# Optimization experiments

Measured on AMD Instinct MI355X. Metric: run time of the kernel, lower is better.

The kernel has to match this reference:

```python
import math
import jax, jax.numpy as jnp
import numpy as np

FNUM = 64      # exp_channels (fnum)
NHEADS = 4     # num_heads
WS = 8         # window size (both spatial dims)
SHIFT = 4      # cyclic shift (hard-coded in module)
SCALE = FNUM ** -0.5   # NOTE: module scales by fnum**-0.5, not head_dim**-0.5
LN_EPS = 1e-5


def sine_pos_encoding(h, w, num_pos_feats, temperature=10000.0):
    # DETR-style normalized sine position encoding -> (1, h*w, 2*num_pos_feats)
    scale = 2.0 * math.pi
    y = np.cumsum(np.ones((1, h, w), dtype=np.float64), axis=1)
    x = np.cumsum(np.ones((1, h, w), dtype=np.float64), axis=2)
    eps = 1e-6
    y = y / (y[:, -1:, :] + eps) * scale
    x = x / (x[:, :, -1:] + eps) * scale
    dim_t = np.arange(num_pos_feats, dtype=np.float64)
    dim_t = temperature ** (2.0 * (dim_t // 2) / num_pos_feats)
    pos_x = x[..., None] / dim_t
    pos_y = y[..., None] / dim_t
    pos_x = np.stack([np.sin(pos_x[..., 0::2]), np.cos(pos_x[..., 1::2])], axis=-1).reshape(1, h, w, -1)
    pos_y = np.stack([np.sin(pos_y[..., 0::2]), np.cos(pos_y[..., 1::2])], axis=-1).reshape(1, h, w, -1)
    pos = np.concatenate([pos_y, pos_x], axis=-1)
    return jnp.asarray(pos.reshape(1, h * w, 2 * num_pos_feats), dtype=jnp.float32)


def compute_mask_np(H, W, ws, ss):
    # Swin shifted-window attention mask -> (nW, ws*ws, ws*ws) with 0 / -100
    img = np.zeros((H, W))
    cnt = 0
    for hs in (slice(0, -ws), slice(-ws, -ss), slice(-ss, None)):
        for wsl in (slice(0, -ws), slice(-ws, -ss), slice(-ss, None)):
            img[hs, wsl] = cnt
            cnt += 1
    mw = img.reshape(H // ws, ws, W // ws, ws).transpose(0, 2, 1, 3).reshape(-1, ws * ws)
    diff = mw[:, None, :] - mw[:, :, None]
    return jnp.asarray(np.where(diff != 0, -100.0, 0.0), dtype=jnp.float32)


def layernorm(x, w, b):
    m = x.mean(-1, keepdims=True)
    v = x.var(-1, keepdims=True)
    return (x - m) * jax.lax.rsqrt(v + LN_EPS) * w + b


def window_attention(q, k, v, mask):
    # q,k,v: (Bw, nH, N, Ch); mask: (nW, N, N)
    att = jnp.einsum('bhnc,bhmc->bhnm', q * SCALE, k)
    nW, N = mask.shape[0], mask.shape[1]
    att = att.reshape(-1, nW, NHEADS, N, N) + mask[None, :, None]
    att = jax.nn.softmax(att.reshape(-1, NHEADS, N, N), axis=-1)
    out = jnp.einsum('bhnm,bhmc->bnhc', att, v)   # merge heads as (nH C)
    return out.reshape(out.shape[0], N, -1)


def merge_heads(q):
    # (Bw, nH, N, Ch) -> (Bw, N, nH*Ch)
    return q.transpose(0, 2, 1, 3).reshape(q.shape[0], q.shape[2], -1)


def geglu(h, w11, b11, w12, b12, w2, b2):
    return (jax.nn.gelu(h @ w11 + b11, approximate=False) * (h @ w12 + b12)) @ w2 + b2


def reference(x, ln1_w, ln1_b, ln2_w, ln2_b, w_qkv, me_w11, me_b11, me_w12, me_b12, me_w2, me_b2, conv11_w, ff_in_w, ff_dw_w, ff_out_w):
    B, _, C, H, W = x.shape
    nHw, nWw = H // WS, W // WS
    nW = nHw * nWw
    N = WS * WS
    Ch = FNUM // NHEADS
    pos = sine_pos_encoding(WS, WS, FNUM // 2)
    mask = compute_mask_np(H, W, WS, SHIFT)
    x0 = x
    xs = jnp.roll(x, (-SHIFT, -SHIFT), axis=(3, 4))
    # window partition: (B,3,C,H,W) -> (B*3*nW, N, C)
    xw = xs.reshape(B, 3, C, nHw, WS, nWw, WS).transpose(0, 1, 3, 5, 4, 6, 2).reshape(-1, N, C)
    xw = layernorm(xw, ln1_w, ln1_b)
    qkv = (xw + pos) @ w_qkv                                   # (B*3*nW, N, 3F)
    # '(B E nW) W (nP C) -> E nP (B nW) W C'
    qkv = qkv.reshape(B, 3, nW, N, 3, FNUM).transpose(1, 4, 0, 2, 3, 5).reshape(3, 3, B * nW, N, FNUM)
    # '(C nH)' head split: head index is the fast axis (faithful to source)
    qkv = qkv.reshape(3, 3, B * nW, N, Ch, NHEADS).transpose(0, 1, 2, 5, 3, 4)  # (E, P, Bw, nH, N, Ch)
    a1 = window_attention(qkv[1, 0], qkv[0, 1], qkv[0, 2], mask)
    a3 = window_attention(qkv[1, 0], qkv[2, 1], qkv[2, 2], mask)
    a21 = window_attention(qkv[0, 0], qkv[1, 1], qkv[1, 2], mask)
    a21b = window_attention(qkv[0, 0], qkv[2, 1], qkv[2, 2], mask)
    a23 = window_attention(qkv[2, 0], qkv[1, 1], qkv[1, 2], mask)
    a23b = window_attention(qkv[2, 0], qkv[0, 1], qkv[0, 2], mask)
    # keep_query=True path: concat attended features with own query, GEGLU per exposure
    h1 = geglu(jnp.concatenate([a21, a21b, merge_heads(qkv[0, 0])], -1), me_w11[0], me_b11[0], me_w12[0], me_b12[0], me_w2[0], me_b2[0])
    h2 = geglu(jnp.concatenate([a1, a3, merge_heads(qkv[1, 0])], -1), me_w11[1], me_b11[1], me_w12[1], me_b12[1], me_w2[1], me_b2[1])
    h3 = geglu(jnp.concatenate([a23, a23b, merge_heads(qkv[2, 0])], -1), me_w11[2], me_b11[2], me_w12[2], me_b12[2], me_w2[2], me_b2[2])
    xc = jnp.concatenate([h1, h2, h3], 0)                      # (3*B*nW, N, F)
    # window reverse + ffn_dconv 1x1 conv across 3F channels
    xr = xc.reshape(3, B, nHw, nWw, WS, WS, FNUM).transpose(1, 0, 6, 2, 4, 3, 5).reshape(B, 3 * FNUM, H, W)
    xr = jnp.einsum('oi,bihw->bohw', conv11_w, xr).reshape(B, 3, FNUM, H, W)
    xr = jnp.roll(xr, (SHIFT, SHIFT), axis=(3, 4))
    xres = xr + x0
    # FFN: LN over (N C), then GEGLU dwconv FeedForward
    xl = layernorm(xres.transpose(0, 3, 4, 1, 2).reshape(B, H, W, 3 * FNUM), ln2_w, ln2_b)
    xcn = xl.transpose(0, 3, 1, 2)                             # (B, 3F, H, W)
    h = jnp.einsum('oi,bihw->bohw', ff_in_w, xcn)              # (B, 12F, H, W)
    h = jax.lax.conv_general_dilated(h, ff_dw_w[:, None], (1, 1), ((1, 1), (1, 1)),
                                     feature_group_count=h.shape[1],
                                     dimension_numbers=('NCHW', 'OIHW', 'NCHW'))
    g1, g2 = jnp.split(h, 2, axis=1)
    h = jax.nn.gelu(g1, approximate=False) * g2                # (B, 6F, H, W)
    out = jnp.einsum('oi,bihw->bohw', ff_out_w, h).reshape(B, 3, FNUM, H, W)
    return xres + out


def setup_inputs():
    key = jax.random.key(0)
    ks = jax.random.split(key, 10)
    F3, F6, F12 = 3 * FNUM, 6 * FNUM, 12 * FNUM
    def w(k, shape, fan_in):
        return jax.random.normal(k, shape, jnp.float32) * (fan_in ** -0.5)
    return {
        'x': jax.random.normal(ks[0], (1, 3, FNUM, 256, 256), jnp.float32),
        'ln1_w': jnp.ones((FNUM,), jnp.float32),
        'ln1_b': jnp.zeros((FNUM,), jnp.float32),
        'ln2_w': jnp.ones((F3,), jnp.float32),
        'ln2_b': jnp.zeros((F3,), jnp.float32),
        'w_qkv': w(ks[1], (FNUM, F3), FNUM),
        'me_w11': w(ks[2], (3, F3, FNUM), F3),
        'me_b11': jnp.zeros((3, FNUM), jnp.float32),
        'me_w12': w(ks[3], (3, F3, FNUM), F3),
        'me_b12': jnp.zeros((3, FNUM), jnp.float32),
        'me_w2': w(ks[4], (3, FNUM, FNUM), FNUM),
        'me_b2': jnp.zeros((3, FNUM), jnp.float32),
        'conv11_w': w(ks[5], (F3, F3), F3),
        'ff_in_w': w(ks[6], (F12, F3), F3),
        'ff_dw_w': w(ks[7], (F12, 3, 3), 9),
        'ff_out_w': w(ks[8], (F3, F6), F6),
    }
```

## Files before the change

kernel.cpp:

```cpp
#include <hip/hip_runtime.h>
#include <hip/hip_bf16.h>
#include <math.h>

typedef __hip_bfloat16 bf16;
typedef __attribute__((ext_vector_type(8))) short short8;
typedef __attribute__((ext_vector_type(4))) short short4v;
typedef __attribute__((ext_vector_type(4))) float f32x4;

__device__ __forceinline__ float b2f(bf16 v) { return __bfloat162float(v); }
__device__ __forceinline__ bf16 f2b(float v) { return __float2bfloat16(v); }
__device__ __forceinline__ short f2s(float v) { bf16 b = __float2bfloat16(v); return *(short*)&b; }
__device__ __forceinline__ float s2f(short s) { bf16 b = *(bf16*)&s; return __bfloat162float(b); }
__device__ __forceinline__ float gelu_exact(float x) {
  return 0.5f * x * (1.0f + erff(x * 0.7071067811865476f));
}
__device__ __forceinline__ bool detect_f32(const void* ln1w) {
  return *(const unsigned int*)ln1w == 0x3F800000u;
}
__device__ __forceinline__ float ldx(const void* p, int i, bool f32) {
  return f32 ? ((const float*)p)[i] : b2f(((const bf16*)p)[i]);
}
#define MFMA16(a, b, c) __builtin_amdgcn_mfma_f32_16x16x32_bf16((a), (b), (c), 0, 0, 0)

#define OFF_LN1W  0
#define OFF_LN1B  64
#define OFF_LN2W  128
#define OFF_LN2B  320
#define OFF_WQKVT 512
#define OFF_W11T  12800
#define OFF_B11   49664
#define OFF_W12T  49856
#define OFF_B12   86720
#define OFF_W2T   86912
#define OFF_B2    99200
#define OFF_CW    99392
#define OFF_FIW   136256
#define OFF_DWW   283712
#define OFF_FOW   290624

__global__ void __launch_bounds__(256) k_convert(
    const void* __restrict__ src, bf16* __restrict__ dst, int n,
    const void* __restrict__ raw) {
  const bool f32 = detect_f32(raw);
  int i = blockIdx.x * 256 + threadIdx.x;
  if (i < n) dst[i] = f2b(ldx(src, i, f32));
}

__global__ void __launch_bounds__(256) k_convT(
    const void* __restrict__ src, bf16* __restrict__ dst, int R, int C, int n,
    const void* __restrict__ raw) {
  const bool f32 = detect_f32(raw);
  int i = blockIdx.x * 256 + threadIdx.x;
  if (i >= n) return;
  int rc = R * C;
  int s = i / rc, rem = i - s * rc;
  int r = rem / C, c = rem - r * C;
  dst[s * rc + c * R + r] = f2b(ldx(src, i, f32));
}

__global__ void __launch_bounds__(256) k_pos(float* __restrict__ posT) {
  int i = blockIdx.x * 256 + threadIdx.x;
  if (i >= 4096) return;
  int t = i >> 6, ch = i & 63;
  int r = t >> 3, c = t & 7;
  int c2 = ch & 31;
  float coord = (ch < 32) ? (float)(r + 1) : (float)(c + 1);
  float base = coord * (6.283185307179586f / 8.000001f);
  int k = c2 >> 1;
  float d = powf(10000.0f, (float)k * (1.0f / 16.0f));
  float a = base / d;
  posT[i] = (c2 & 1) ? cosf(a) : sinf(a);
}

__global__ void __launch_bounds__(256) k_qkv(
    const void* __restrict__ x, const void* __restrict__ raw,
    const bf16* __restrict__ W, const float* __restrict__ posT,
    short* __restrict__ qkvS, int wy0, int NWL) {
  const int wl = blockIdx.x;
  const int wy = wy0 + (wl >> 5), wx = wl & 31;
  const int tid = threadIdx.x;
  const bool xf32 = detect_f32(raw);

  __shared__ alignas(16) short xln[192 * 72];
  __shared__ alignas(16) short qout[64 * 200];
  __shared__ float mu[192], rs[192];

  for (int i = tid; i < 3072; i += 256) {
    int xq = i & 1, ty = (i >> 1) & 7, ch = (i >> 4) & 63, e = i >> 10;
    int y  = (wy * 8 + ty + 4) & 255;
    int xs = (wx * 8 + 4 + xq * 4) & 255;
    size_t gi = ((size_t)(e * 64 + ch) * 256 + y) * 256 + xs;
    float f0, f1, f2, f3;
    if (xf32) {
      f32x4 v4 = *(const f32x4*)((const float*)x + gi);
      f0 = v4[0]; f1 = v4[1]; f2 = v4[2]; f3 = v4[3];
    } else {
      short4v v4 = *(const short4v*)((const bf16*)x + gi);
      f0 = s2f(v4[0]); f1 = s2f(v4[1]); f2 = s2f(v4[2]); f3 = s2f(v4[3]);
    }
    int tb = (e * 64 + ty * 8 + xq * 4) * 72 + ch;
    xln[tb]       = f2s(f0);
    xln[tb + 72]  = f2s(f1);
    xln[tb + 144] = f2s(f2);
    xln[tb + 216] = f2s(f3);
  }
  __syncthreads();
  if (tid < 192) {
    const short* row = xln + tid * 72;
    float s = 0.f, s2 = 0.f;
    #pragma unroll
    for (int k8 = 0; k8 < 8; k8++) {
      short8 v = *(const short8*)(row + k8 * 8);
      #pragma unroll
      for (int j = 0; j < 8; j++) { float f = s2f(v[j]); s += f; s2 += f * f; }
    }
    float m = s * (1.0f / 64.0f);
    float var = s2 * (1.0f / 64.0f) - m * m;
    mu[tid] = m; rs[tid] = rsqrtf(var + 1e-5f);
  }
  __syncthreads();
  for (int u = tid; u < 1536; u += 256) {
    int co = u & 7, t = (u >> 3) & 63, e = u >> 9;
    int idx = (e * 64 + t) * 72 + co * 8;
    short8 xv = *(const short8*)(xln + idx);
    float m = mu[e * 64 + t], rr = rs[e * 64 + t];
    const float* pt = posT + t * 64 + co * 8;
    f32x4 pa = *(const f32x4*)pt;
    f32x4 pb = *(const f32x4*)(pt + 4);
    short8 lw = *(const short8*)(const void*)(W + OFF_LN1W + co * 8);
    short8 lb = *(const short8*)(const void*)(W + OFF_LN1B + co * 8);
    short8 o;
    #pragma unroll
    for (int j = 0; j < 8; j++) {
      float p = (j < 4) ? pa[j] : pb[j - 4];
      o[j] = f2s((s2f(xv[j]) - m) * rr * s2f(lw[j]) + s2f(lb[j]) + p);
    }
    *(short8*)(xln + idx) = o;
  }
  __syncthreads();

  const int lid = tid & 63;
  const int w = tid >> 6;
  const int mrow = lid & 15, q = lid >> 4;
  const bf16* wqT = W + OFF_WQKVT;
  for (int e = 0; e < 3; e++) {
    short8 a0 = *(const short8*)(xln + (e * 64 + w * 16 + mrow) * 72 + q * 8);
    short8 a1 = *(const short8*)(xln + (e * 64 + w * 16 + mrow) * 72 + 32 + q * 8);
    for (int nt = 0; nt < 12; nt++) {
      f32x4 acc = {0.f, 0.f, 0.f, 0.f};
      short8 b0 = *(const short8*)(const void*)(wqT + (nt * 16 + mrow) * 64 + q * 8);
      short8 b1 = *(const short8*)(const void*)(wqT + (nt * 16 + mrow) * 64 + 32 + q * 8);
      acc = MFMA16(a0, b0, acc);
      acc = MFMA16(a1, b1, acc);
      #pragma unroll
      for (int r = 0; r < 4; r++)
        qout[(w * 16 + q * 4 + r) * 200 + nt * 16 + mrow] = f2s(acc[r]);
    }
    __syncthreads();
    for (int i = tid; i < 3072; i += 256) {
      int p = i >> 10, rem = i & 1023;
      int tt = rem >> 4, f4 = (rem & 15) * 4;
      *(short4v*)(qkvS + ((size_t)wl * 9 + e * 3 + p) * 4096 + tt * 64 + f4)
          = *(const short4v*)(qout + tt * 200 + p * 64 + f4);
    }
    __syncthreads();
  }
}

__global__ void __launch_bounds__(256, 3) k_attn(
    const short* __restrict__ qkvS, const bf16* __restrict__ W,
    short* __restrict__ xcS, int wy0, int NWL) {
  const int e  = blockIdx.x / NWL;
  const int wl = blockIdx.x - e * NWL;
  const int wy = wy0 + (wl >> 5), wx = wl & 31;
  const int tid = threadIdx.x;

  __shared__ alignas(16) short cat[64 * 200];
  __shared__ alignas(16) short Kh[4 * 64 * 16];
  __shared__ alignas(16) short Vt[4 * 16 * 72];
  __shared__ alignas(16) short Pb[64 * 72];
  short* gbuf = Pb;

  const int ea = (e == 0) ? 1 : ((e == 1) ? 0 : 1);
  const int eb = (e == 0) ? 2 : ((e == 1) ? 2 : 0);
  const short* Qg = qkvS + ((size_t)wl * 9 + e * 3 + 0) * 4096;
  const short* Kg[2] = { qkvS + ((size_t)wl * 9 + ea * 3 + 1) * 4096,
                         qkvS + ((size_t)wl * 9 + eb * 3 + 1) * 4096 };
  const short* Vg[2] = { qkvS + ((size_t)wl * 9 + ea * 3 + 2) * 4096,
                         qkvS + ((size_t)wl * 9 + eb * 3 + 2) * 4096 };

  for (int i = tid; i < 512; i += 256) {
    int t = i >> 3, chunk = i & 7;
    short8 v = *(const short8*)(Qg + t * 64 + chunk * 8);
    #pragma unroll
    for (int j = 0; j < 8; j++) {
      int f = chunk * 8 + j;
      cat[t * 200 + 128 + (f & 3) * 16 + (f >> 2)] = v[j];
    }
  }

  const int lid = tid & 63;
  const int w = tid >> 6;
  const int mrow = lid & 15, q = lid >> 4;
  const int masky = (wy == 31), maskx = (wx == 31);
  const short8 zero8 = {0, 0, 0, 0, 0, 0, 0, 0};

  for (int src = 0; src < 2; src++) {
    if (src) __syncthreads();
    for (int i = tid; i < 512; i += 256) {
      int t = i >> 3, chunk = i & 7;
      short8 v = *(const short8*)(Kg[src] + t * 64 + chunk * 8);
      #pragma unroll
      for (int j = 0; j < 8; j++) {
        int f = chunk * 8 + j;
        Kh[((f & 3) * 64 + t) * 16 + (f >> 2)] = v[j];
      }
    }
    for (int i = tid; i < 512; i += 256) {
      int t = i & 63, chunk = i >> 6;
      short8 v = *(const short8*)(Vg[src] + t * 64 + chunk * 8);
      #pragma unroll
      for (int j = 0; j < 8; j++) {
        int f = chunk * 8 + j;
        Vt[((f & 3) * 16 + (f >> 2)) * 72 + t] = v[j];
      }
    }
    __syncthreads();

    for (int h = 0; h < 4; h++) {
      short8 af = (q < 2)
          ? *(const short8*)(cat + (w * 16 + mrow) * 200 + 128 + h * 16 + q * 8) : zero8;
      f32x4 s[4];
      #pragma unroll
      for (int nt = 0; nt < 4; nt++) {
        short8 bfr = (q < 2)
            ? *(const short8*)(Kh + (h * 64 + nt * 16 + mrow) * 16 + q * 8) : zero8;
        f32x4 acc = {0.f, 0.f, 0.f, 0.f};
        s[nt] = MFMA16(af, bfr, acc);
      }
      #pragma unroll
      for (int nt = 0; nt < 4; nt++) {
        int kj = nt * 16 + mrow;
        int lyj = masky ? (((kj >> 3) < 4) ? 1 : 2) : 0;
        int lxj = maskx ? (((kj & 7) < 4) ? 1 : 2) : 0;
        #pragma unroll
        for (int r = 0; r < 4; r++) {
          int qi = w * 16 + q * 4 + r;
          int lyi = masky ? (((qi >> 3) < 4) ? 1 : 2) : 0;
          int lxi = maskx ? (((qi & 7) < 4) ? 1 : 2) : 0;
          float sv = s[nt][r] * 0.125f;
          if (lyi != lyj || lxi != lxj) sv -= 100.0f;
          s[nt][r] = sv;
        }
      }
      #pragma unroll
      for (int r = 0; r < 4; r++) {
        float mx = fmaxf(fmaxf(s[0][r], s[1][r]), fmaxf(s[2][r], s[3][r]));
        mx = fmaxf(mx, __shfl_xor(mx, 1));
        mx = fmaxf(mx, __shfl_xor(mx, 2));
        mx = fmaxf(mx, __shfl_xor(mx, 4));
        mx = fmaxf(mx, __shfl_xor(mx, 8));
        float p0 = __expf(s[0][r] - mx), p1 = __expf(s[1][r] - mx);
        float p2 = __expf(s[2][r] - mx), p3 = __expf(s[3][r] - mx);
        float sum = (p0 + p1) + (p2 + p3);
        sum += __shfl_xor(sum, 1);
        sum += __shfl_xor(sum, 2);
        sum += __shfl_xor(sum, 4);
        sum += __shfl_xor(sum, 8);
        float inv = 1.0f / sum;
        int ro = (w * 16 + q * 4 + r) * 72;
        Pb[ro + mrow]      = f2s(p0 * inv);
        Pb[ro + 16 + mrow] = f2s(p1 * inv);
        Pb[ro + 32 + mrow] = f2s(p2 * inv);
        Pb[ro + 48 + mrow] = f2s(p3 * inv);
      }
      asm volatile("s_waitcnt lgkmcnt(0)" ::: "memory");
      f32x4 o = {0.f, 0.f, 0.f, 0.f};
      #pragma unroll
      for (int kc = 0; kc < 2; kc++) {
        short8 pa = *(const short8*)(Pb + (w * 16 + mrow) * 72 + kc * 32 + q * 8);
        short8 vb = *(const short8*)(Vt + (h * 16 + mrow) * 72 + kc * 32 + q * 8);
        o = MFMA16(pa, vb, o);
      }
      #pragma unroll
      for (int r = 0; r < 4; r++)
        cat[(w * 16 + q * 4 + r) * 200 + src * 64 + h * 16 + mrow] = f2s(o[r]);
    }
  }
  __syncthreads();

  {
    short8 a[6];
    #pragma unroll
    for (int kc = 0; kc < 6; kc++)
      a[kc] = *(const short8*)(cat + (w * 16 + mrow) * 200 + kc * 32 + q * 8);
    f32x4 ua[4], va[4];
    const bf16* w1T = W + OFF_W11T + (size_t)e * 64 * 192;
    const bf16* w2T = W + OFF_W12T + (size_t)e * 64 * 192;
    for (int nt = 0; nt < 4; nt++) {
      f32x4 au = {0.f, 0.f, 0.f, 0.f}, av = {0.f, 0.f, 0.f, 0.f};
      #pragma unroll
      for (int kc = 0; kc < 6; kc++) {
        short8 bu = *(const short8*)(const void*)(w1T + (nt * 16 + mrow) * 192 + kc * 32 + q * 8);
        short8 bv = *(const short8*)(const void*)(w2T + (nt * 16 + mrow) * 192 + kc * 32 + q * 8);
        au = MFMA16(a[kc], bu, au);
        av = MFMA16(a[kc], bv, av);
      }
      ua[nt] = au; va[nt] = av;
    }
    for (int nt = 0; nt < 4; nt++) {
      int o = nt * 16 + mrow;
      float bu = b2f(W[OFF_B11 + e * 64 + o]);
      float bv = b2f(W[OFF_B12 + e * 64 + o]);
      #pragma unroll
      for (int r = 0; r < 4; r++)
        gbuf[(w * 16 + q * 4 + r) * 72 + o] = f2s(gelu_exact(ua[nt][r] + bu) * (va[nt][r] + bv));
    }
  }
  {
    short8 g0 = *(const short8*)(gbuf + (w * 16 + mrow) * 72 + q * 8);
    short8 g1 = *(const short8*)(gbuf + (w * 16 + mrow) * 72 + 32 + q * 8);
    const bf16* w2T = W + OFF_W2T + (size_t)e * 64 * 64;
    for (int nt = 0; nt < 4; nt++) {
      f32x4 acc = {0.f, 0.f, 0.f, 0.f};
      short8 b0 = *(const short8*)(const void*)(w2T + (nt * 16 + mrow) * 64 + q * 8);
      short8 b1 = *(const short8*)(const void*)(w2T + (nt * 16 + mrow) * 64 + 32 + q * 8);
      acc = MFMA16(g0, b0, acc);
      acc = MFMA16(g1, b1, acc);
      int o = nt * 16 + mrow;
      float bb = b2f(W[OFF_B2 + e * 64 + o]);
      #pragma unroll
      for (int r = 0; r < 4; r++)
        cat[(w * 16 + q * 4 + r) * 200 + o] = f2s(acc[r] + bb);
    }
  }
  __syncthreads();
  short* xcbase = xcS + ((size_t)wl * 3 + e) * 4096;
  for (int i = tid; i < 1024; i += 256) {
    int tt = i >> 4, f4 = (i & 15) * 4;
    *(short4v*)(xcbase + tt * 64 + f4) = *(const short4v*)(cat + tt * 200 + f4);
  }
}

__global__ void __launch_bounds__(256) k_conv11(
    const short* __restrict__ xcS, const bf16* __restrict__ W,
    const void* __restrict__ x, const void* __restrict__ raw,
    short* __restrict__ xres, int wy0, int NWL) {
  const int wl = blockIdx.x;
  const int wy = wy0 + (wl >> 5), wx = wl & 31;
  const int tid = threadIdx.x;
  const bool xf32 = detect_f32(raw);
  __shared__ alignas(16) short ct[64 * 200];
  __shared__ alignas(16) short xt[64 * 200];

  for (int i = tid; i < 3072; i += 256) {
    int e = i >> 10, rem = i & 1023;
    int tt = rem >> 4, f4 = (rem & 15) * 4;
    *(short4v*)(ct + tt * 200 + e * 64 + f4)
        = *(const short4v*)(xcS + ((size_t)wl * 3 + e) * 4096 + tt * 64 + f4);
  }
  for (int i = tid; i < 3072; i += 256) {
    int xq = i & 1, ty = (i >> 1) & 7, ch = (i >> 4) & 63, e = i >> 10;
    int y  = (wy * 8 + ty + 4) & 255;
    int xs = (wx * 8 + 4 + xq * 4) & 255;
    size_t gi = ((size_t)(e * 64 + ch) * 256 + y) * 256 + xs;
    float f0, f1, f2, f3;
    if (xf32) {
      f32x4 v4 = *(const f32x4*)((const float*)x + gi);
      f0 = v4[0]; f1 = v4[1]; f2 = v4[2]; f3 = v4[3];
    } else {
      short4v v4 = *(const short4v*)((const bf16*)x + gi);
      f0 = s2f(v4[0]); f1 = s2f(v4[1]); f2 = s2f(v4[2]); f3 = s2f(v4[3]);
    }
    int tb = (ty * 8 + xq * 4) * 200 + e * 64 + ch;
    xt[tb]       = f2s(f0);
    xt[tb + 200] = f2s(f1);
    xt[tb + 400] = f2s(f2);
    xt[tb + 600] = f2s(f3);
  }
  __syncthreads();

  const int lid = tid & 63;
  const int w = tid >> 6;
  const int mrow = lid & 15, q = lid >> 4;
  short8 a[6];
  #pragma unroll
  for (int kc = 0; kc < 6; kc++)
    a[kc] = *(const short8*)(ct + (w * 16 + mrow) * 200 + kc * 32 + q * 8);
  __syncthreads();

  const bf16* cw = W + OFF_CW;
  for (int nt = 0; nt < 12; nt++) {
    f32x4 acc = {0.f, 0.f, 0.f, 0.f};
    #pragma unroll
    for (int kc = 0; kc < 6; kc++) {
      short8 b = *(const short8*)(const void*)(cw + (nt * 16 + mrow) * 192 + kc * 32 + q * 8);
      acc = MFMA16(a[kc], b, acc);
    }
    int o = nt * 16 + mrow;
    #pragma unroll
    for (int r = 0; r < 4; r++) {
      int t = w * 16 + q * 4 + r;
      ct[t * 200 + o] = f2s(acc[r] + s2f(xt[t * 200 + o]));
    }
  }
  __syncthreads();
  for (int i4 = tid; i4 < 3072; i4 += 256) {
    int t = i4 / 48, o4 = (i4 - t * 48) * 4;
    int y  = (wy * 8 + (t >> 3) + 4) & 255;
    int xx = (wx * 8 + (t & 7) + 4) & 255;
    *(short4v*)(xres + (size_t)(y * 256 + xx) * 192 + o4)
        = *(const short4v*)(ct + t * 200 + o4);
  }
}

__global__ void __launch_bounds__(256) k_ffin(
    const short* __restrict__ xres, const bf16* __restrict__ W,
    short* __restrict__ hS, int y_start, int y0m1) {
  const int y = y_start + (blockIdx.x >> 2);
  const int x0 = (blockIdx.x & 3) * 64;
  const int l = y - y0m1;
  const int tid = threadIdx.x;
  __shared__ alignas(16) short xt[64 * 200];
  __shared__ float mu[64], rs[64];

  for (int i4 = tid; i4 < 3072; i4 += 256) {
    int p = i4 / 48, c4 = (i4 - p * 48) * 4;
    *(short4v*)(xt + p * 200 + c4)
        = *(const short4v*)(xres + (size_t)(y * 256 + x0 + p) * 192 + c4);
  }
  __syncthreads();
  {
    int p = tid >> 2, qd = tid & 3;
    const short* row = xt + p * 200 + qd * 48;
    float s = 0.f, s2 = 0.f;
    #pragma unroll
    for (int k = 0; k < 6; k++) {
      short8 v = *(const short8*)(row + k * 8);
      #pragma unroll
      for (int j = 0; j < 8; j++) { float f = s2f(v[j]); s += f; s2 += f * f; }
    }
    s  += __shfl_xor(s, 1);  s  += __shfl_xor(s, 2);
    s2 += __shfl_xor(s2, 1); s2 += __shfl_xor(s2, 2);
    if (qd == 0) {
      float m = s * (1.0f / 192.0f);
      float var = s2 * (1.0f / 192.0f) - m * m;
      mu[p] = m; rs[p] = rsqrtf(var + 1e-5f);
    }
  }
  __syncthreads();
  for (int i = tid; i < 12288; i += 256) {
    int p = i & 63, ch = i >> 6;
    int idx = p * 200 + ch;
    xt[idx] = f2s((s2f(xt[idx]) - mu[p]) * rs[p] * b2f(W[OFF_LN2W + ch]) + b2f(W[OFF_LN2B + ch]));
  }
  __syncthreads();

  const int lid = tid & 63;
  const int m0 = (tid >> 6) * 16;
  const int mrow = lid & 15, q = lid >> 4;
  short8 a[6];
  #pragma unroll
  for (int kc = 0; kc < 6; kc++)
    a[kc] = *(const short8*)(xt + (m0 + mrow) * 200 + kc * 32 + q * 8);
  __syncthreads();

  const bf16* fiw = W + OFF_FIW;
  for (int c = 0; c < 4; c++) {
    for (int j = 0; j < 12; j++) {
      int nt = c * 12 + j;
      f32x4 acc = {0.f, 0.f, 0.f, 0.f};
      #pragma unroll
      for (int kc = 0; kc < 6; kc++) {
        short8 b = *(const short8*)(const void*)(fiw + (nt * 16 + mrow) * 192 + kc * 32 + q * 8);
        acc = MFMA16(a[kc], b, acc);
      }
      #pragma unroll
      for (int r = 0; r < 4; r++)
        xt[(m0 + q * 4 + r) * 200 + j * 16 + mrow] = f2s(acc[r]);
    }
    __syncthreads();
    for (int i4 = tid; i4 < 3072; i4 += 256) {
      int t = i4 / 48, o4 = (i4 - t * 48) * 4;
      *(short4v*)(hS + (size_t)l * 196608 + (size_t)(x0 + t) * 768 + c * 192 + o4)
          = *(const short4v*)(xt + t * 200 + o4);
    }
    __syncthreads();
  }
}

__global__ void __launch_bounds__(256) k_ffout(
    const short* __restrict__ hS, const bf16* __restrict__ W,
    const short* __restrict__ xres, void* __restrict__ out,
    const void* __restrict__ raw, int y0, int y0m1) {
  const int y = y0 + (blockIdx.x >> 2);
  const int x0 = (blockIdx.x & 3) * 64;
  const int tid = threadIdx.x;
  const bool of32 = detect_f32(raw);
  __shared__ alignas(16) short ga[64 * 392];

  const bf16* dwwT = W + OFF_DWW;
  const int l = y - y0m1;
  const short8 z8 = {0, 0, 0, 0, 0, 0, 0, 0};
  for (int it = 0; it < 6; it++) {
    int unit = it * 256 + tid;
    int pq = unit / 48, oo = unit - pq * 48;
    int o = oo * 8;
    int xxb = x0 + pq * 2;
    float u0[8] = {0,0,0,0,0,0,0,0}, v0[8] = {0,0,0,0,0,0,0,0};
    float u1[8] = {0,0,0,0,0,0,0,0}, v1[8] = {0,0,0,0,0,0,0,0};
    #pragma unroll
    for (int dy = -1; dy <= 1; dy++) {
      int yy = y + dy;
      if (yy < 0 || yy >= 256) continue;
      const short* rbase = hS + (size_t)(l + dy) * 196608;
      short8 hu[4], hv[4];
      #pragma unroll
      for (int k = 0; k < 4; k++) {
        int xv = xxb - 1 + k;
        if (xv < 0 || xv >= 256) { hu[k] = z8; hv[k] = z8; }
        else {
          const short* hp = rbase + (size_t)xv * 768 + o;
          hu[k] = *(const short8*)(hp);
          hv[k] = *(const short8*)(hp + 384);
        }
      }
      const bf16* wrow = dwwT + (dy + 1) * 3 * 768 + o;
      short8 w0u = *(const short8*)(const void*)(wrow);
      short8 w0v = *(const short8*)(const void*)(wrow + 384);
      short8 w1u = *(const short8*)(const void*)(wrow + 768);
      short8 w1v = *(const short8*)(const void*)(wrow + 768 + 384);
      short8 w2u = *(const short8*)(const void*)(wrow + 1536);
      short8 w2v = *(const short8*)(const void*)(wrow + 1536 + 384);
      #pragma unroll
      for (int j = 0; j < 8; j++) {
        float a0 = s2f(w0u[j]), a1 = s2f(w1u[j]), a2 = s2f(w2u[j]);
        float b0 = s2f(w0v[j]), b1 = s2f(w1v[j]), b2 = s2f(w2v[j]);
        float h0u = s2f(hu[0][j]), h1u = s2f(hu[1][j]), h2u = s2f(hu[2][j]), h3u = s2f(hu[3][j]);
        float h0v = s2f(hv[0][j]), h1v = s2f(hv[1][j]), h2v = s2f(hv[2][j]), h3v = s2f(hv[3][j]);
        u0[j] += a0 * h0u + a1 * h1u + a2 * h2u;
        u1[j] += a0 * h1u + a1 * h2u + a2 * h3u;
        v0[j] += b0 * h0v + b1 * h1v + b2 * h2v;
        v1[j] += b0 * h1v + b1 * h2v + b2 * h3v;
      }
    }
    short8 g0, g1;
    #pragma unroll
    for (int j = 0; j < 8; j++) {
      g0[j] = f2s(gelu_exact(u0[j]) * v0[j]);
      g1[j] = f2s(gelu_exact(u1[j]) * v1[j]);
    }
    *(short8*)(ga + (pq * 2) * 392 + o)     = g0;
    *(short8*)(ga + (pq * 2 + 1) * 392 + o) = g1;
  }
  __syncthreads();

  const int lid = tid & 63;
  const int m0 = (tid >> 6) * 16;
  const int mrow = lid & 15, q = lid >> 4;
  short8 a[12];
  #pragma unroll
  for (int kc = 0; kc < 12; kc++)
    a[kc] = *(const short8*)(ga + (m0 + mrow) * 392 + kc * 32 + q * 8);
  __syncthreads();

  for (int i4 = tid; i4 < 3072; i4 += 256) {
    int pp = i4 / 48, c4 = (i4 - pp * 48) * 4;
    *(short4v*)(ga + pp * 392 + 200 + c4)
        = *(const short4v*)(xres + (size_t)(y * 256 + x0 + pp) * 192 + c4);
  }

  const bf16* fow = W + OFF_FOW;
  for (int nt = 0; nt < 12; nt++) {
    f32x4 acc = {0.f, 0.f, 0.f, 0.f};
    #pragma unroll
    for (int kc = 0; kc < 12; kc++) {
      short8 b = *(const short8*)(const void*)(fow + (nt * 16 + mrow) * 384 + kc * 32 + q * 8);
      acc = MFMA16(a[kc], b, acc);
    }
    #pragma unroll
    for (int r = 0; r < 4; r++)
      ga[(m0 + q * 4 + r) * 392 + nt * 16 + mrow] = f2s(acc[r]);
  }
  __syncthreads();

  for (int it = 0; it < 48; it++) {
    int flat = it * 256 + tid;
    int pp = flat & 63, ch = flat >> 6;
    int idx = ch * 65536 + y * 256 + x0 + pp;
    float r = s2f(ga[pp * 392 + ch]) + s2f(ga[pp * 392 + 200 + ch]);
    if (of32) ((float*)out)[idx] = r;
    else      ((bf16*)out)[idx] = f2b(r);
  }
}

extern "C" void kernel_launch(void* const* d_in, const int* in_sizes, int n_in,
                              void* d_out, int out_size, void* d_ws, size_t ws_size,
                              hipStream_t stream) {
  const void* x   = d_in[0];
  const void* raw = d_in[1];
  char* ws = (char*)d_ws;
  bf16*  W    = (bf16*)(ws + 1024);
  float* posT = (float*)(ws + 786432);
  short* xres = (short*)(ws + 0x100000);
  const size_t ATT = 28ull * 1024 * 1024;

  size_t avail = (ws_size > ATT) ? ws_size - ATT : 0;
  int swr = 32;
  while (swr > 1 && (size_t)swr * 3145728ull > avail) swr >>= 1;
  int hr = 256;
  while (hr > 4 && (size_t)(hr + 2) * 393216ull > avail) hr >>= 1;

  short* qkvS = (short*)(ws + ATT);
  short* xcS  = (short*)(ws + ATT + (size_t)swr * 2359296ull);
  short* hS   = (short*)(ws + ATT);

  { const int di[10]   = {1, 2, 3, 4, 7, 9, 11, 12, 13, 15};
    const int offp[10] = {OFF_LN1W, OFF_LN1B, OFF_LN2W, OFF_LN2B, OFF_B11,
                          OFF_B12, OFF_B2, OFF_CW, OFF_FIW, OFF_FOW};
    const int cnt[10]  = {64, 64, 192, 192, 192, 192, 192, 36864, 147456, 73728};
    for (int i = 0; i < 10; i++)
      k_convert<<<(cnt[i] + 255) / 256, 256, 0, stream>>>(
          d_in[di[i]], W + offp[i], cnt[i], raw);
  }
  k_convT<<<(12288 + 255) / 256, 256, 0, stream>>>(d_in[5], W + OFF_WQKVT, 64, 192, 12288, raw);
  k_convT<<<(36864 + 255) / 256, 256, 0, stream>>>(d_in[6], W + OFF_W11T, 192, 64, 36864, raw);
  k_convT<<<(36864 + 255) / 256, 256, 0, stream>>>(d_in[8], W + OFF_W12T, 192, 64, 36864, raw);
  k_convT<<<(12288 + 255) / 256, 256, 0, stream>>>(d_in[10], W + OFF_W2T, 64, 64, 12288, raw);
  k_convT<<<(6912 + 255) / 256, 256, 0, stream>>>(d_in[14], W + OFF_DWW, 768, 9, 6912, raw);
  k_pos<<<16, 256, 0, stream>>>(posT);

  for (int wy0 = 0; wy0 < 32; wy0 += swr) {
    int NWL = swr * 32;
    k_qkv<<<NWL, 256, 0, stream>>>(x, raw, W, posT, qkvS, wy0, NWL);
    k_attn<<<3 * NWL, 256, 0, stream>>>(qkvS, W, xcS, wy0, NWL);
    k_conv11<<<NWL, 256, 0, stream>>>(xcS, W, x, raw, xres, wy0, NWL);
  }

  for (int y0 = 0; y0 < 256; y0 += hr) {
    int ys = (y0 == 0) ? 0 : (y0 - 1);
    int ye = (y0 + hr > 255) ? 255 : (y0 + hr);
    int nrows = ye - ys + 1;
    k_ffin<<<nrows * 4, 256, 0, stream>>>(xres, W, hS, ys, y0 - 1);
    k_ffout<<<hr * 4, 256, 0, stream>>>(hS, W, xres, d_out, raw, y0, y0 - 1);
  }
}
```

Before: 741.8 us.

## Pre-layout QKV per head for attention, transpose score MFMA, widen depthwise tiles

The QKV kernel now writes Q, K (pre-scaled by 0.125) and V in head-split, attention-ready layouts, so the attention kernel can copy them with vector loads instead of scalar scatter transposes. Attention computes the transposed score product, so each lane holds a full query row. That turns the softmax reductions into two shuffles and lets probabilities be stored as short4 vectors. The shift mask is precomputed once per thread and applied only on edge windows. Separately, the depthwise FFN stage computes four output pixels per thread instead of two to reuse loaded neighbours, with launch bounds set for three blocks per SM, at the cost of higher register pressure.

```diff
diff --git a/kernel.cpp b/kernel.cpp
--- a/kernel.cpp
+++ b/kernel.cpp
@@ -38,6 +38,10 @@
 #define OFF_DWW   283712
 #define OFF_FOW   290624
 
+#define QOFF 0
+#define KOFF 4352
+#define VOFF 9472
+
 __global__ void __launch_bounds__(256) k_convert(
     const void* __restrict__ src, bf16* __restrict__ dst, int n,
     const void* __restrict__ raw) {
@@ -82,7 +86,7 @@
   const bool xf32 = detect_f32(raw);
 
   __shared__ alignas(16) short xln[192 * 72];
-  __shared__ alignas(16) short qout[64 * 200];
+  __shared__ alignas(16) short qout[13824];
   __shared__ float mu[192], rs[192];
 
   for (int i = tid; i < 3072; i += 256) {
@@ -142,6 +146,8 @@
   const int lid = tid & 63;
   const int w = tid >> 6;
   const int mrow = lid & 15, q = lid >> 4;
+  const int t0 = w * 16 + q * 4;
+  const int h = mrow & 3;
   const bf16* wqT = W + OFF_WQKVT;
   for (int e = 0; e < 3; e++) {
     short8 a0 = *(const short8*)(xln + (e * 64 + w * 16 + mrow) * 72 + q * 8);
@@ -152,16 +158,33 @@
       short8 b1 = *(const short8*)(const void*)(wqT + (nt * 16 + mrow) * 64 + 32 + q * 8);
       acc = MFMA16(a0, b0, acc);
       acc = MFMA16(a1, b1, acc);
-      #pragma unroll
-      for (int r = 0; r < 4; r++)
-        qout[(w * 16 + q * 4 + r) * 200 + nt * 16 + mrow] = f2s(acc[r]);
+      int p = nt >> 2;
+      int c = (nt & 3) * 4 + (mrow >> 2);
+      if (p == 0) {
+        int o2 = h * 16 + c;
+        #pragma unroll
+        for (int r = 0; r < 4; r++)
+          qout[QOFF + (t0 + r) * 68 + o2] = f2s(acc[r]);
+      } else if (p == 1) {
+        int rb = KOFF + (h * 64 + t0) * 20 + c;
+        #pragma unroll
+        for (int r = 0; r < 4; r++)
+          qout[rb + r * 20] = f2s(acc[r] * 0.125f);
+      } else {
+        int rb = VOFF + (h * 16 + c) * 68 + q * 16 + w;
+        #pragma unroll
+        for (int r = 0; r < 4; r++)
+          qout[rb + r * 4] = f2s(acc[r]);
+      }
     }
     __syncthreads();
-    for (int i = tid; i < 3072; i += 256) {
-      int p = i >> 10, rem = i & 1023;
-      int tt = rem >> 4, f4 = (rem & 15) * 4;
-      *(short4v*)(qkvS + ((size_t)wl * 9 + e * 3 + p) * 4096 + tt * 64 + f4)
-          = *(const short4v*)(qout + tt * 200 + p * 64 + f4);
+    const size_t gb = ((size_t)wl * 9 + e * 3) * 4096;
+    for (int u = tid; u < 3072; u += 256) {
+      int j = u * 4, p = j >> 12, rem = j & 4095, src;
+      if (p == 0)      src = QOFF + (rem >> 6) * 68 + (rem & 63);
+      else if (p == 1) src = KOFF + (rem >> 4) * 20 + (rem & 15);
+      else             src = VOFF + (rem >> 6) * 68 + (rem & 63);
+      *(short4v*)(qkvS + gb + j) = *(const short4v*)(qout + src);
     }
     __syncthreads();
   }
@@ -176,9 +199,10 @@
   const int tid = threadIdx.x;
 
   __shared__ alignas(16) short cat[64 * 200];
-  __shared__ alignas(16) short Kh[4 * 64 * 16];
-  __shared__ alignas(16) short Vt[4 * 16 * 72];
+  __shared__ alignas(16) short Kh[4096];
+  __shared__ alignas(16) short Vt[64 * 72];
   __shared__ alignas(16) short Pb[64 * 72];
+  __shared__ alignas(16) short kz[16];
   short* gbuf = Pb;
 
   const int ea = (e == 0) ? 1 : ((e == 1) ? 0 : 1);
@@ -189,90 +213,89 @@
   const short* Vg[2] = { qkvS + ((size_t)wl * 9 + ea * 3 + 2) * 4096,
                          qkvS + ((size_t)wl * 9 + eb * 3 + 2) * 4096 };
 
+  if (tid < 16) kz[tid] = 0;
   for (int i = tid; i < 512; i += 256) {
-    int t = i >> 3, chunk = i & 7;
-    short8 v = *(const short8*)(Qg + t * 64 + chunk * 8);
-    #pragma unroll
-    for (int j = 0; j < 8; j++) {
-      int f = chunk * 8 + j;
-      cat[t * 200 + 128 + (f & 3) * 16 + (f >> 2)] = v[j];
-    }
+    int t = i >> 3, ch = i & 7;
+    *(short8*)(cat + t * 200 + 128 + ch * 8) = *(const short8*)(Qg + t * 64 + ch * 8);
   }
 
   const int lid = tid & 63;
   const int w = tid >> 6;
   const int mrow = lid & 15, q = lid >> 4;
   const int masky = (wy == 31), maskx = (wx == 31);
+  const bool anymask = (masky | maskx) != 0;
   const short8 zero8 = {0, 0, 0, 0, 0, 0, 0, 0};
+
+  float madd[4][4];
+  if (anymask) {
+    int qi = w * 16 + mrow;
+    int lyi = masky ? (((qi >> 3) < 4) ? 1 : 2) : 0;
+    int lxi = maskx ? (((qi & 7) < 4) ? 1 : 2) : 0;
+    #pragma unroll
+    for (int nt = 0; nt < 4; nt++)
+      #pragma unroll
+      for (int r = 0; r < 4; r++) {
+        int kj = nt * 16 + q * 4 + r;
+        int lyj = masky ? (((kj >> 3) < 4) ? 1 : 2) : 0;
+        int lxj = maskx ? (((kj & 7) < 4) ? 1 : 2) : 0;
+        madd[nt][r] = (lyi != lyj || lxi != lxj) ? -100.0f : 0.0f;
+      }
+  }
 
   for (int src = 0; src < 2; src++) {
     if (src) __syncthreads();
+    for (int i = tid; i < 512; i += 256)
+      *(short8*)(Kh + i * 8) = *(const short8*)(Kg[src] + i * 8);
     for (int i = tid; i < 512; i += 256) {
-      int t = i >> 3, chunk = i & 7;
-      short8 v = *(const short8*)(Kg[src] + t * 64 + chunk * 8);
-      #pragma unroll
-      for (int j = 0; j < 8; j++) {
-        int f = chunk * 8 + j;
-        Kh[((f & 3) * 64 + t) * 16 + (f >> 2)] = v[j];
-      }
-    }
-    for (int i = tid; i < 512; i += 256) {
-      int t = i & 63, chunk = i >> 6;
-      short8 v = *(const short8*)(Vg[src] + t * 64 + chunk * 8);
-      #pragma unroll
-      for (int j = 0; j < 8; j++) {
-        int f = chunk * 8 + j;
-        Vt[((f & 3) * 16 + (f >> 2)) * 72 + t] = v[j];
-      }
+      int row = i >> 3, ch = i & 7;
+      *(short8*)(Vt + row * 72 + ch * 8) = *(const short8*)(Vg[src] + row * 64 + ch * 8);
     }
     __syncthreads();
 
     for (int h = 0; h < 4; h++) {
-      short8 af = (q < 2)
-          ? *(const short8*)(cat + (w * 16 + mrow) * 200 + 128 + h * 16 + q * 8) : zero8;
+      short8 qf = (q < 2)
+          ? *(const short8*)(cat + (w * 16 + mrow) * 200 + 128 + h * 16 + q * 8)
+          : zero8;
+      const short* kb; int kstep;
+      if (q < 2) { kb = Kh + (h * 64 + mrow) * 16 + q * 8; kstep = 256; }
+      else       { kb = kz; kstep = 0; }
       f32x4 s[4];
       #pragma unroll
       for (int nt = 0; nt < 4; nt++) {
-        short8 bfr = (q < 2)
-            ? *(const short8*)(Kh + (h * 64 + nt * 16 + mrow) * 16 + q * 8) : zero8;
-        f32x4 acc = {0.f, 0.f, 0.f, 0.f};
-        s[nt] = MFMA16(af, bfr, acc);
-      }
-      #pragma unroll
-      for (int nt = 0; nt < 4; nt++) {
-        int kj = nt * 16 + mrow;
-        int lyj = masky ? (((kj >> 3) < 4) ? 1 : 2) : 0;
-        int lxj = maskx ? (((kj & 7) < 4) ? 1 : 2) : 0;
+        short8 kf = *(const short8*)(kb + nt * kstep);
+        f32x4 z = {0.f, 0.f, 0.f, 0.f};
+        s[nt] = MFMA16(kf, qf, z);
+      }
+      if (anymask) {
+        #pragma unroll
+        for (int nt = 0; nt < 4; nt++)
+          #pragma unroll
+          for (int r = 0; r < 4; r++) s[nt][r] += madd[nt][r];
+      }
+      float mx = s[0][0];
+      #pragma unroll
+      for (int nt = 0; nt < 4; nt++)
+        #pragma unroll
+        for (int r = 0; r < 4; r++) if (nt | r) mx = fmaxf(mx, s[nt][r]);
+      mx = fmaxf(mx, __shfl_xor(mx, 16));
+      mx = fmaxf(mx, __shfl_xor(mx, 32));
+      float pr[4][4]; float sum = 0.f;
+      #pragma unroll
+      for (int nt = 0; nt < 4; nt++)
         #pragma unroll
         for (int r = 0; r < 4; r++) {
-          int qi = w * 16 + q * 4 + r;
-          int lyi = masky ? (((qi >> 3) < 4) ? 1 : 2) : 0;
-          int lxi = maskx ? (((qi & 7) < 4) ? 1 : 2) : 0;
-          float sv = s[nt][r] * 0.125f;
-          if (lyi != lyj || lxi != lxj) sv -= 100.0f;
-          s[nt][r] = sv;
+          float ev = __expf(s[nt][r] - mx);
+          pr[nt][r] = ev; sum += ev;
         }
-      }
+      sum += __shfl_xor(sum, 16);
+      sum += __shfl_xor(sum, 32);
+      float inv = 1.0f / sum;
+      int ro = (w * 16 + mrow) * 72 + q * 16;
       #pragma unroll
       for (int r = 0; r < 4; r++) {
-        float mx = fmaxf(fmaxf(s[0][r], s[1][r]), fmaxf(s[2][r], s[3][r]));
-        mx = fmaxf(mx, __shfl_xor(mx, 1));
-        mx = fmaxf(mx, __shfl_xor(mx, 2));
-        mx = fmaxf(mx, __shfl_xor(mx, 4));
-        mx = fmaxf(mx, __shfl_xor(mx, 8));
-        float p0 = __expf(s[0][r] - mx), p1 = __expf(s[1][r] - mx);
-        float p2 = __expf(s[2][r] - mx), p3 = __expf(s[3][r] - mx);
-        float sum = (p0 + p1) + (p2 + p3);
-        sum += __shfl_xor(sum, 1);
-        sum += __shfl_xor(sum, 2);
-        sum += __shfl_xor(sum, 4);
-        sum += __shfl_xor(sum, 8);
-        float inv = 1.0f / sum;
-        int ro = (w * 16 + q * 4 + r) * 72;
-        Pb[ro + mrow]      = f2s(p0 * inv);
-        Pb[ro + 16 + mrow] = f2s(p1 * inv);
-        Pb[ro + 32 + mrow] = f2s(p2 * inv);
-        Pb[ro + 48 + mrow] = f2s(p3 * inv);
+        short4v pv = { f2s(pr[0][r] * inv), f2s(pr[1][r] * inv),
+                       f2s(pr[2][r] * inv), f2s(pr[3][r] * inv) };
+        *(short4v*)(Pb + ro + r * 4) = pv;
       }
       asm volatile("s_waitcnt lgkmcnt(0)" ::: "memory");
       f32x4 o = {0.f, 0.f, 0.f, 0.f};
@@ -489,7 +512,7 @@
   }
 }
 
-__global__ void __launch_bounds__(256) k_ffout(
+__global__ void __launch_bounds__(256, 3) k_ffout(
     const short* __restrict__ hS, const bf16* __restrict__ W,
     const short* __restrict__ xres, void* __restrict__ out,
     const void* __restrict__ raw, int y0, int y0m1) {
@@ -502,21 +525,24 @@
   const bf16* dwwT = W + OFF_DWW;
   const int l = y - y0m1;
   const short8 z8 = {0, 0, 0, 0, 0, 0, 0, 0};
-  for (int it = 0; it < 6; it++) {
+  for (int it = 0; it < 3; it++) {
     int unit = it * 256 + tid;
     int pq = unit / 48, oo = unit - pq * 48;
     int o = oo * 8;
-    int xxb = x0 + pq * 2;
-    float u0[8] = {0,0,0,0,0,0,0,0}, v0[8] = {0,0,0,0,0,0,0,0};
-    float u1[8] = {0,0,0,0,0,0,0,0}, v1[8] = {0,0,0,0,0,0,0,0};
+    int xxb = x0 + pq * 4;
+    float u[4][8], v[4][8];
+    #pragma unroll
+    for (int t4 = 0; t4 < 4; t4++)
+      #pragma unroll
+      for (int j = 0; j < 8; j++) { u[t4][j] = 0.f; v[t4][j] = 0.f; }
     #pragma unroll
     for (int dy = -1; dy <= 1; dy++) {
       int yy = y + dy;
       if (yy < 0 || yy >= 256) continue;
       const short* rbase = hS + (size_t)(l + dy) * 196608;
-      short8 hu[4], hv[4];
-      #pragma unroll
-      for (int k = 0; k < 4; k++) {
+      short8 hu[6], hv[6];
+      #pragma unroll
+      for (int k = 0; k < 6; k++) {
         int xv = xxb - 1 + k;
         if (xv < 0 || xv >= 256) { hu[k] = z8; hv[k] = z8; }
         else {
@@ -536,22 +562,27 @@
       for (int j = 0; j < 8; j++) {
         float a0 = s2f(w0u[j]), a1 = s2f(w1u[j]), a2 = s2f(w2u[j]);
         float b0 = s2f(w0v[j]), b1 = s2f(w1v[j]), b2 = s2f(w2v[j]);
-        float h0u = s2f(hu[0][j]), h1u = s2f(hu[1][j]), h2u = s2f(hu[2][j]), h3u = s2f(hu[3][j]);
-        float h0v = s2f(hv[0][j]), h1v = s2f(hv[1][j]), h2v = s2f(hv[2][j]), h3v = s2f(hv[3][j]);
-        u0[j] += a0 * h0u + a1 * h1u + a2 * h2u;
-        u1[j] += a0 * h1u + a1 * h2u + a2 * h3u;
-        v0[j] += b0 * h0v + b1 * h1v + b2 * h2v;
-        v1[j] += b0 * h1v + b1 * h2v + b2 * h3v;
-      }
-    }
-    short8 g0, g1;
-    #pragma unroll
-    for (int j = 0; j < 8; j++) {
-      g0[j] = f2s(gelu_exact(u0[j]) * v0[j]);
-      g1[j] = f2s(gelu_exact(u1[j]) * v1[j]);
-    }
-    *(short8*)(ga + (pq * 2) * 392 + o)     = g0;
-    *(short8*)(ga + (pq * 2 + 1) * 392 + o) = g1;
+        float fu0 = s2f(hu[0][j]), fu1 = s2f(hu[1][j]), fu2 = s2f(hu[2][j]);
+        float fu3 = s2f(hu[3][j]), fu4 = s2f(hu[4][j]), fu5 = s2f(hu[5][j]);
+        float fv0 = s2f(hv[0][j]), fv1 = s2f(hv[1][j]), fv2 = s2f(hv[2][j]);
+        float fv3 = s2f(hv[3][j]), fv4 = s2f(hv[4][j]), fv5 = s2f(hv[5][j]);
+        u[0][j] += a0 * fu0 + a1 * fu1 + a2 * fu2;
+        u[1][j] += a0 * fu1 + a1 * fu2 + a2 * fu3;
+        u[2][j] += a0 * fu2 + a1 * fu3 + a2 * fu4;
+        u[3][j] += a0 * fu3 + a1 * fu4 + a2 * fu5;
+        v[0][j] += b0 * fv0 + b1 * fv1 + b2 * fv2;
+        v[1][j] += b0 * fv1 + b1 * fv2 + b2 * fv3;
+        v[2][j] += b0 * fv2 + b1 * fv3 + b2 * fv4;
+        v[3][j] += b0 * fv3 + b1 * fv4 + b2 * fv5;
+      }
+    }
+    #pragma unroll
+    for (int t4 = 0; t4 < 4; t4++) {
+      short8 g;
+      #pragma unroll
+      for (int j = 0; j < 8; j++) g[j] = f2s(gelu_exact(u[t4][j]) * v[t4][j]);
+      *(short8*)(ga + (pq * 4 + t4) * 392 + o) = g;
+    }
   }
   __syncthreads();
 
```

Result: slower. 757.4 us (+2.1%).
